# Performance work log

Hardware: AMD Instinct MI355X
Metric: run time of the kernel (lower is better)

## Reference

```python
import jax, jax.numpy as jnp
import numpy as np
import math

N_HEAD = 16
V_HEAD = 32   # v_head_dim
NOPE = 32     # nope_head_dim
ROPE_D = 64   # rope_head_dim
KEEP = 256    # num_tokens_to_keep
EPS = 1e-6


def _freqs(T, dim=ROPE_D, theta=10000.0):
    f = 1.0 / (theta ** (jnp.arange(0, dim, 2, dtype=jnp.float32) / dim))
    t = jnp.arange(T, dtype=jnp.float32)
    a = jnp.outer(t, f)  # [T, dim//2]
    return jnp.cos(a), jnp.sin(a)


def _rope(x, cos, sin):
    # x: [B,H,S,D]; half-split rotation as in apply_rope
    S = x.shape[-2]
    c = cos[:S][None, None]
    s = sin[:S][None, None]
    x1, x2 = jnp.split(x, 2, axis=-1)
    return jnp.concatenate([x1 * c - x2 * s, x1 * s + x2 * c], axis=-1)


def _rms(x, g, eps=EPS):
    return x * jax.lax.rsqrt(jnp.mean(x * x, axis=-1, keepdims=True) + eps) * g


def _attn(q, k, v, causal):
    scale = 1.0 / math.sqrt(q.shape[-1])
    s = jnp.einsum('bhqd,bhkd->bhqk', q, k) * scale
    if causal:
        Tq, Tk = s.shape[-2], s.shape[-1]
        mask = jnp.tril(jnp.ones((Tq, Tk), dtype=bool))
        s = jnp.where(mask, s, jnp.finfo(s.dtype).min)
    return jnp.einsum('bhqk,bhkd->bhqd', jax.nn.softmax(s, axis=-1), v)


def _forward(x, w_cq, g_qnorm, w_dq_nope, w_dq_rope, w_ckv, g_kvnorm,
             w_dk_nope, w_dv, w_krope, w_imp, w_selk, w_selv,
             w_wink, w_winv, w_gate, w_proj):
    B, T, C = x.shape
    cos, sin = _freqs(T)

    # --- MLA query path ---
    nq = _rms(x @ w_cq, g_qnorm)                                  # [B,T,96]
    q_nope = (nq @ w_dq_nope).reshape(B, T, N_HEAD, NOPE).transpose(0, 2, 1, 3)
    q_rope = (nq @ w_dq_rope).reshape(B, T, N_HEAD, ROPE_D).transpose(0, 2, 1, 3)
    q_rope = _rope(q_rope, cos, sin)
    q = jnp.concatenate([q_nope, q_rope], axis=-1)                # [B,H,T,96]

    # --- branch gate ---
    gate = jax.nn.softmax((x @ w_gate).mean(axis=1), axis=-1)     # [B,3]

    # --- branch 1: MLA-compressed full KV ---
    ckv = _rms(x @ w_ckv, g_kvnorm)                               # [B,T,32]
    k_nope = (ckv @ w_dk_nope).reshape(B, T, N_HEAD, NOPE).transpose(0, 2, 1, 3)
    v1 = (ckv @ w_dv).reshape(B, T, N_HEAD, V_HEAD).transpose(0, 2, 1, 3)
    k_rope = (x @ w_krope).reshape(B, T, 1, ROPE_D).transpose(0, 2, 1, 3) / N_HEAD
    k_rope = _rope(k_rope, cos, sin)
    k1 = jnp.concatenate(
        [k_nope, jnp.broadcast_to(k_rope, (B, N_HEAD, T, ROPE_D))], axis=-1)

    # --- branch 2: top-k selected tokens ---
    scores = (x @ w_imp)[..., 0]                                  # [B,T]
    _, idx = jax.lax.top_k(scores, KEEP)
    idx = jnp.sort(idx, axis=1)
    sel = jnp.take_along_axis(x, idx[:, :, None], axis=1)         # [B,S,C]
    ks = (sel @ w_selk).reshape(B, KEEP, N_HEAD, NOPE + ROPE_D).transpose(0, 2, 1, 3)
    vs = (sel @ w_selv).reshape(B, KEEP, N_HEAD, V_HEAD).transpose(0, 2, 1, 3)
    ks = jnp.concatenate([ks[..., :NOPE], _rope(ks[..., NOPE:], cos, sin)], axis=-1)

    # --- branch 3: sliding window (training mode -> full x) ---
    kw = (x @ w_wink).reshape(B, T, N_HEAD, NOPE + ROPE_D).transpose(0, 2, 1, 3)
    vw = (x @ w_winv).reshape(B, T, N_HEAD, V_HEAD).transpose(0, 2, 1, 3)
    kw = jnp.concatenate([kw[..., :NOPE], _rope(kw[..., NOPE:], cos, sin)], axis=-1)

    a1 = _attn(q, k1, v1, causal=True)
    a2 = _attn(q, ks, vs, causal=False)
    a3 = _attn(q, kw, vw, causal=True)

    g = gate[:, :, None, None, None]
    out = g[:, 0] * a1 + g[:, 1] * a2 + g[:, 2] * a3              # [B,H,T,Vd]
    out = out.transpose(0, 2, 1, 3).reshape(B, T, N_HEAD * V_HEAD)
    return out @ w_proj                                           # [B,T,C]


def setup_inputs() -> dict:
    key = jax.random.key(0)
    ks = jax.random.split(key, 20)
    B, T, C = 2, 1024, 1024
    q_lora, kv_lora = 96, 32
    std = 0.02
    def w(k, shape):
        return jax.random.normal(k, shape, dtype=jnp.float32) * std
    return {
        'x': jax.random.normal(ks[0], (B, T, C), dtype=jnp.float32),
        'w_cq': w(ks[1], (C, q_lora)),
        'g_qnorm': jnp.ones((q_lora,), jnp.float32),
        'w_dq_nope': w(ks[2], (q_lora, N_HEAD * NOPE)),
        'w_dq_rope': w(ks[3], (q_lora, N_HEAD * ROPE_D)),
        'w_ckv': w(ks[4], (C, kv_lora)),
        'g_kvnorm': jnp.ones((kv_lora,), jnp.float32),
        'w_dk_nope': w(ks[5], (kv_lora, N_HEAD * NOPE)),
        'w_dv': w(ks[6], (kv_lora, N_HEAD * V_HEAD)),
        'w_krope': w(ks[7], (C, ROPE_D)),
        'w_imp': w(ks[8], (C, 1)),
        'w_selk': w(ks[9], (C, N_HEAD * (NOPE + ROPE_D))),
        'w_selv': w(ks[10], (C, N_HEAD * V_HEAD)),
        'w_wink': w(ks[11], (C, N_HEAD * (NOPE + ROPE_D))),
        'w_winv': w(ks[12], (C, N_HEAD * V_HEAD)),
        'w_gate': w(ks[13], (C, 3)),
        'w_proj': w(ks[14], (N_HEAD * V_HEAD, C)),
    }


def reference(x, w_cq, g_qnorm, w_dq_nope, w_dq_rope, w_ckv, g_kvnorm,
              w_dk_nope, w_dv, w_krope, w_imp, w_selk, w_selv,
              w_wink, w_winv, w_gate, w_proj):
    return _forward(x, w_cq, g_qnorm, w_dq_nope, w_dq_rope, w_ckv, g_kvnorm,
                    w_dk_nope, w_dv, w_krope, w_imp, w_selk, w_selv,
                    w_wink, w_winv, w_gate, w_proj)
```

## Files before the change

kernel.cpp:

```cpp
#include <hip/hip_runtime.h>
#include <math.h>

#define T_SEQ   1024
#define BATCH   2
#define CDIM    1024
#define NHEAD   16
#define VHEAD   32
#define KEEP    256
#define HEAD_D  96
#define SCALE_ATTN 0.1020620726159658f

#define BQ   64
#define BKT  64
#define SK   100
#define SPT  66
#define SPV  36

#define GBK 16
#define SA  132

#define XWW    2244
#define C_CQ   0
#define C_CKV  96
#define C_KRO  128
#define C_WINK 192
#define C_WINV 1728
#define C_IMP  2240
#define C_GATE 2241

#define QKVW   2560
#define C_QN   0
#define C_QR   512
#define C_KN   1536
#define C_V1   2048

#define SKW  2048

__global__ __launch_bounds__(256) void gemm128(const float* __restrict__ A,
                                               const float* __restrict__ B,
                                               float* __restrict__ C,
                                               int M, int N, int K,
                                               int lda, int ldb, int ldc,
                                               int kchunk,
                                               const int* __restrict__ Arowidx,
                                               int rowdiv, int rowmul) {
    __shared__ float As[GBK][SA];
    __shared__ float Bs[GBK][SA];
    int t = threadIdx.x;
    int tx = t & 15, ty = t >> 4;
    int row0 = blockIdx.y * 128, col0 = blockIdx.x * 128;
    int kb = blockIdx.z * kchunk;
    int ke = min(K, kb + kchunk);
    float acc[8][8] = {};

    int asrc[2]; bool aok[2];
#pragma unroll
    for (int r = 0; r < 2; r++) {
        int idx = t + 256 * r;
        int row = idx >> 2;
        int gr = row0 + row;
        aok[r] = (gr < M);
        int ar = gr;
        if (Arowidx != nullptr && aok[r]) ar = (gr / rowdiv) * rowmul + Arowidx[gr];
        asrc[r] = ar;
    }

    for (int k0 = kb; k0 < ke; k0 += GBK) {
#pragma unroll
        for (int r = 0; r < 2; r++) {
            int idx = t + 256 * r;
            int row = idx >> 2, k4 = idx & 3;
            float4 v = make_float4(0.f, 0.f, 0.f, 0.f);
            if (aok[r]) v = *(const float4*)&A[(size_t)asrc[r] * lda + k0 + k4 * 4];
            As[k4 * 4 + 0][row] = v.x;
            As[k4 * 4 + 1][row] = v.y;
            As[k4 * 4 + 2][row] = v.z;
            As[k4 * 4 + 3][row] = v.w;
        }
#pragma unroll
        for (int r = 0; r < 2; r++) {
            int idx = t + 256 * r;
            int kk = idx >> 5, n4 = idx & 31;
            int gc = col0 + n4 * 4;
            float4 v = make_float4(0.f, 0.f, 0.f, 0.f);
            if (gc + 3 < N) {
                v = *(const float4*)&B[(size_t)(k0 + kk) * ldb + gc];
            } else if (gc < N) {
                const float* bp = &B[(size_t)(k0 + kk) * ldb];
                float tmp[4] = {0.f, 0.f, 0.f, 0.f};
                for (int j = 0; j < 4 && gc + j < N; j++) tmp[j] = bp[gc + j];
                v = make_float4(tmp[0], tmp[1], tmp[2], tmp[3]);
            }
            *(float4*)&Bs[kk][n4 * 4] = v;
        }
        __syncthreads();
#pragma unroll
        for (int kk = 0; kk < GBK; kk++) {
            float4 a0 = *(float4*)&As[kk][ty * 4];
            float4 a1 = *(float4*)&As[kk][64 + ty * 4];
            float4 b0 = *(float4*)&Bs[kk][tx * 4];
            float4 b1 = *(float4*)&Bs[kk][64 + tx * 4];
            float av[8] = {a0.x, a0.y, a0.z, a0.w, a1.x, a1.y, a1.z, a1.w};
            float bv[8] = {b0.x, b0.y, b0.z, b0.w, b1.x, b1.y, b1.z, b1.w};
#pragma unroll
            for (int i = 0; i < 8; i++)
#pragma unroll
                for (int j = 0; j < 8; j++) acc[i][j] += av[i] * bv[j];
        }
        __syncthreads();
    }

    bool split = (gridDim.z > 1);
#pragma unroll
    for (int i = 0; i < 8; i++) {
        int gr = row0 + ((i < 4) ? (ty * 4 + i) : (64 + ty * 4 + (i - 4)));
        if (gr >= M) continue;
#pragma unroll
        for (int half = 0; half < 2; half++) {
            int gc = col0 + half * 64 + tx * 4;
            if (gc + 3 >= N) continue;
            float* cp = &C[(size_t)gr * ldc + gc];
            if (split) {
                atomicAdd(cp + 0, acc[i][half * 4 + 0]);
                atomicAdd(cp + 1, acc[i][half * 4 + 1]);
                atomicAdd(cp + 2, acc[i][half * 4 + 2]);
                atomicAdd(cp + 3, acc[i][half * 4 + 3]);
            } else {
                *(float4*)cp = make_float4(acc[i][half * 4 + 0], acc[i][half * 4 + 1],
                                           acc[i][half * 4 + 2], acc[i][half * 4 + 3]);
            }
        }
    }
}

__global__ void pack_all(float* __restrict__ Bxw, float* __restrict__ Bqkv,
                         float* __restrict__ Bsel, float2* __restrict__ tab,
                         const float* __restrict__ cq, const float* __restrict__ ckv,
                         const float* __restrict__ kro, const float* __restrict__ wink,
                         const float* __restrict__ winv, const float* __restrict__ imp,
                         const float* __restrict__ gate,
                         const float* __restrict__ dqn, const float* __restrict__ dqr,
                         const float* __restrict__ dkn, const float* __restrict__ dv,
                         const float* __restrict__ selk, const float* __restrict__ selv) {
    int blk = blockIdx.x;
    if (blk < 1024) {
        int r = blk;
        for (int c = threadIdx.x; c < XWW; c += blockDim.x) {
            float v;
            if      (c < C_CKV)  v = cq  [(size_t)r * 96   + c];
            else if (c < C_KRO)  v = ckv [(size_t)r * 32   + (c - C_CKV)];
            else if (c < C_WINK) v = kro [(size_t)r * 64   + (c - C_KRO)];
            else if (c < C_WINV) v = wink[(size_t)r * 1536 + (c - C_WINK)];
            else if (c < C_IMP)  v = winv[(size_t)r * 512  + (c - C_WINV)];
            else if (c < C_GATE) v = imp [(size_t)r * 1    + (c - C_IMP)];
            else                 v = gate[(size_t)r * 3    + (c - C_GATE)];
            Bxw[(size_t)r * XWW + c] = v;
        }
    } else if (blk < 1152) {
        int r = blk - 1024;
        for (int c = threadIdx.x; c < QKVW; c += blockDim.x) {
            float v = 0.f;
            if (r < 96) {
                if (c < C_QR)      v = dqn[(size_t)r * 512 + c];
                else if (c < C_KN) v = dqr[(size_t)r * 1024 + (c - C_QR)];
            } else {
                if (c >= C_KN && c < C_V1) v = dkn[(size_t)(r - 96) * 512 + (c - C_KN)];
                else if (c >= C_V1)        v = dv [(size_t)(r - 96) * 512 + (c - C_V1)];
            }
            Bqkv[(size_t)r * QKVW + c] = v;
        }
    } else if (blk < 2176) {
        int r = blk - 1152;
        for (int c = threadIdx.x; c < SKW; c += blockDim.x) {
            float v = (c < 1536) ? selk[(size_t)r * 1536 + c]
                                 : selv[(size_t)r * 512 + (c - 1536)];
            Bsel[(size_t)r * SKW + c] = v;
        }
    } else {
        int idx = (blk - 2176) * 256 + threadIdx.x;
        if (idx < T_SEQ * 32) {
            int pos = idx >> 5, i = idx & 31;
            float expo = (float)i * (1.0f / 32.0f);
            float f = 1.0f / powf(10000.0f, expo);
            float a = (float)pos * f;
            float s, c;
            sincosf(a, &s, &c);
            tab[idx] = make_float2(c, s);
        }
    }
}

__global__ void xw_post(float* __restrict__ XW, const float* __restrict__ gq,
                        const float* __restrict__ gkv,
                        const float2* __restrict__ tab) {
    int row = blockIdx.x;
    int t = threadIdx.x;
    int w = t >> 6, lane = t & 63;
    float* rp = XW + (size_t)row * XWW;
    int pos = row & (T_SEQ - 1);
    const float2* tp = tab + pos * 32;

    if (w == 0) {
        float ss = 0.f;
        for (int d = lane; d < 96; d += 64) { float v = rp[d]; ss += v * v; }
        for (int off = 32; off; off >>= 1) ss += __shfl_xor(ss, off, 64);
        float r = rsqrtf(ss / 96.0f + 1e-6f);
        for (int d = lane; d < 96; d += 64) rp[d] *= r * gq[d];
    } else if (w == 1) {
        float ss = 0.f;
        for (int d = lane; d < 32; d += 64) { float v = rp[C_CKV + d]; ss += v * v; }
        for (int off = 32; off; off >>= 1) ss += __shfl_xor(ss, off, 64);
        float r = rsqrtf(ss / 32.0f + 1e-6f);
        for (int d = lane; d < 32; d += 64) rp[C_CKV + d] *= r * gkv[d];
    } else if (w == 2) {
        if (lane < 32) {
            float2 cs = tp[lane];
            float v1 = rp[C_KRO + lane], v2 = rp[C_KRO + 32 + lane];
            rp[C_KRO + lane]      = (v1 * cs.x - v2 * cs.y) * (1.0f / NHEAD);
            rp[C_KRO + 32 + lane] = (v1 * cs.y + v2 * cs.x) * (1.0f / NHEAD);
        }
    }
#pragma unroll
    for (int j = 0; j < 2; j++) {
        int item = t + j * 256;
        int h = item >> 5, i = item & 31;
        float2 cs = tp[i];
        size_t base = (size_t)(C_WINK + 32) + h * 96;
        float v1 = rp[base + i], v2 = rp[base + 32 + i];
        rp[base + i]      = v1 * cs.x - v2 * cs.y;
        rp[base + 32 + i] = v1 * cs.y + v2 * cs.x;
    }
}

__global__ void topk_gate(const float* __restrict__ xw, int* __restrict__ idx,
                          float* __restrict__ gate) {
    int b = blockIdx.x;
    __shared__ float s[1024];
    __shared__ int ps[1024];
    __shared__ float gred[3][16];
    int t = threadIdx.x;
    const float* rowp = &xw[((size_t)b * T_SEQ + t) * XWW];
    s[t] = rowp[C_IMP];
    float g0 = rowp[C_GATE + 0], g1 = rowp[C_GATE + 1], g2 = rowp[C_GATE + 2];
    for (int off = 32; off; off >>= 1) {
        g0 += __shfl_xor(g0, off, 64);
        g1 += __shfl_xor(g1, off, 64);
        g2 += __shfl_xor(g2, off, 64);
    }
    if ((t & 63) == 0) { int w = t >> 6; gred[0][w] = g0; gred[1][w] = g1; gred[2][w] = g2; }
    __syncthreads();
    if (t == 0) {
        float v0 = 0.f, v1 = 0.f, v2 = 0.f;
        for (int w = 0; w < 16; w++) { v0 += gred[0][w]; v1 += gred[1][w]; v2 += gred[2][w]; }
        v0 /= (float)T_SEQ; v1 /= (float)T_SEQ; v2 /= (float)T_SEQ;
        float m = fmaxf(v0, fmaxf(v1, v2));
        float e0 = expf(v0 - m), e1 = expf(v1 - m), e2 = expf(v2 - m);
        float ssum = e0 + e1 + e2;
        gate[b * 3 + 0] = e0 / ssum;
        gate[b * 3 + 1] = e1 / ssum;
        gate[b * 3 + 2] = e2 / ssum;
    }
    __syncthreads();
    float mine = s[t];
    int rank = 0;
    for (int j = 0; j < 1024; j++) {
        float v = s[j];
        rank += (v > mine) || (v == mine && j < t);
    }
    int selv = (rank < KEEP) ? 1 : 0;
    ps[t] = selv;
    __syncthreads();
    for (int off = 1; off < 1024; off <<= 1) {
        int add = (t >= off) ? ps[t - off] : 0;
        __syncthreads();
        ps[t] += add;
        __syncthreads();
    }
    if (selv) idx[b * KEEP + ps[t] - 1] = t;
}

__global__ __launch_bounds__(512, 4) void flash_fused(
    const float* __restrict__ qkv, const float* __restrict__ xw,
    const float* __restrict__ skv, const float* __restrict__ gate,
    const float2* __restrict__ tab, float* __restrict__ out) {
    __shared__ float Qs[BQ * SK];
    __shared__ float Ks[BKT * SK];
    __shared__ float Vs[BKT * SPV];
    __shared__ float Pt[BKT * SPT];

    int b = blockIdx.z, h = blockIdx.y;
    int qt = blockIdx.x;
    if (b == 1) qt = (gridDim.x - 1) - qt;
    int q0 = qt * BQ;
    int t = threadIdx.x;
    int tq = t >> 4, tk = t & 15;

    for (int i = t; i < BQ * 24; i += 512) {
        int row = i / 24, d4 = i % 24;
        size_t rq = (size_t)b * T_SEQ + q0 + row;
        float4 v;
        if (d4 < 8) {
            v = *(const float4*)&qkv[rq * QKVW + C_QN + h * 32 + d4 * 4];
        } else {
            const float* qb = &qkv[rq * QKVW + C_QR + h * 64];
            int dd = d4 - 8;
            float4 a = *(const float4*)&qb[dd * 4];
            const float2* tp = tab + (size_t)(q0 + row) * 32;
            if (dd < 8) {
                float4 p = *(const float4*)&qb[(dd + 8) * 4];
                int i0 = dd * 4;
                float2 c0 = tp[i0], c1 = tp[i0 + 1], c2 = tp[i0 + 2], c3 = tp[i0 + 3];
                v = make_float4(a.x * c0.x - p.x * c0.y, a.y * c1.x - p.y * c1.y,
                                a.z * c2.x - p.z * c2.y, a.w * c3.x - p.w * c3.y);
            } else {
                float4 p = *(const float4*)&qb[(dd - 8) * 4];
                int i0 = (dd - 8) * 4;
                float2 c0 = tp[i0], c1 = tp[i0 + 1], c2 = tp[i0 + 2], c3 = tp[i0 + 3];
                v = make_float4(p.x * c0.y + a.x * c0.x, p.y * c1.y + a.y * c1.x,
                                p.z * c2.y + a.z * c2.x, p.w * c3.y + a.w * c3.x);
            }
        }
        *(float4*)&Qs[row * SK + d4 * 4] = v;
    }

    int qq0 = q0 + 2 * tq, qq1 = qq0 + 1;
    float comb[2][2] = {};
    for (int phase = 0; phase < 3; phase++) {
        bool causal = (phase != 1);
        int ntiles = causal ? (qt + 1) : (KEEP / BKT);
        float m0 = -1e30f, m1 = -1e30f, l0 = 0.f, l1 = 0.f;
        float o00 = 0.f, o01 = 0.f, o10 = 0.f, o11 = 0.f;

        for (int kt = 0; kt < ntiles; kt++) {
            int j0 = kt * BKT;
            __syncthreads();

            for (int i = t; i < BKT * 24; i += 512) {
                int row = i / 24, d4 = i % 24;
                int j = j0 + row;
                float4 v;
                if (phase == 0) {
                    size_t rk = (size_t)b * T_SEQ + j;
                    if (d4 < 8) v = *(const float4*)&qkv[rk * QKVW + C_KN + h * 32 + d4 * 4];
                    else        v = *(const float4*)&xw[rk * XWW + C_KRO + (d4 - 8) * 4];
                } else if (phase == 1) {
                    const float* kb2 = &skv[((size_t)b * KEEP + j) * SKW + h * 96];
                    if (d4 < 8) {
                        v = *(const float4*)&kb2[d4 * 4];
                    } else {
                        int dd = d4 - 8;
                        float4 a = *(const float4*)&kb2[d4 * 4];
                        const float2* tp = tab + (size_t)j * 32;
                        if (dd < 8) {
                            float4 p = *(const float4*)&kb2[(d4 + 8) * 4];
                            int i0 = dd * 4;
                            float2 c0 = tp[i0], c1 = tp[i0 + 1], c2 = tp[i0 + 2], c3 = tp[i0 + 3];
                            v = make_float4(a.x * c0.x - p.x * c0.y, a.y * c1.x - p.y * c1.y,
                                            a.z * c2.x - p.z * c2.y, a.w * c3.x - p.w * c3.y);
                        } else {
                            float4 p = *(const float4*)&kb2[(d4 - 8) * 4];
                            int i0 = (dd - 8) * 4;
                            float2 c0 = tp[i0], c1 = tp[i0 + 1], c2 = tp[i0 + 2], c3 = tp[i0 + 3];
                            v = make_float4(p.x * c0.y + a.x * c0.x, p.y * c1.y + a.y * c1.x,
                                            p.z * c2.y + a.z * c2.x, p.w * c3.y + a.w * c3.x);
                        }
                    }
                } else {
                    v = *(const float4*)&xw[((size_t)b * T_SEQ + j) * XWW + C_WINK + h * 96 + d4 * 4];
                }
                *(float4*)&Ks[row * SK + d4 * 4] = v;
            }
            for (int i = t; i < BKT * 8; i += 512) {
                int row = i >> 3, d4 = i & 7;
                int j = j0 + row;
                float4 v;
                if (phase == 0)      v = *(const float4*)&qkv[((size_t)b * T_SEQ + j) * QKVW + C_V1 + h * 32 + d4 * 4];
                else if (phase == 1) v = *(const float4*)&skv[((size_t)b * KEEP  + j) * SKW + 1536 + h * 32 + d4 * 4];
                else                 v = *(const float4*)&xw[((size_t)b * T_SEQ + j) * XWW + C_WINV + h * 32 + d4 * 4];
                *(float4*)&Vs[row * SPV + d4 * 4] = v;
            }
            __syncthreads();

            float s0[4] = {}, s1[4] = {};
#pragma unroll 6
            for (int d = 0; d < HEAD_D; d += 4) {
                float4 qa = *(float4*)&Qs[(2 * tq)     * SK + d];
                float4 qb = *(float4*)&Qs[(2 * tq + 1) * SK + d];
#pragma unroll
                for (int j = 0; j < 4; j++) {
                    float4 kv = *(float4*)&Ks[(16 * j + tk) * SK + d];
                    s0[j] += qa.x * kv.x + qa.y * kv.y + qa.z * kv.z + qa.w * kv.w;
                    s1[j] += qb.x * kv.x + qb.y * kv.y + qb.z * kv.z + qb.w * kv.w;
                }
            }
            float mt0 = -1e30f, mt1 = -1e30f;
#pragma unroll
            for (int j = 0; j < 4; j++) {
                int kk = j0 + 16 * j + tk;
                s0[j] *= SCALE_ATTN;
                s1[j] *= SCALE_ATTN;
                if (causal && kk > qq0) s0[j] = -1e30f;
                if (causal && kk > qq1) s1[j] = -1e30f;
                mt0 = fmaxf(mt0, s0[j]);
                mt1 = fmaxf(mt1, s1[j]);
            }
#pragma unroll
            for (int off = 1; off <= 8; off <<= 1) {
                mt0 = fmaxf(mt0, __shfl_xor(mt0, off, 64));
                mt1 = fmaxf(mt1, __shfl_xor(mt1, off, 64));
            }
            float mn0 = fmaxf(m0, mt0), mn1 = fmaxf(m1, mt1);
            float a0 = __expf(m0 - mn0), a1 = __expf(m1 - mn1);
            m0 = mn0; m1 = mn1;

            float rs0 = 0.f, rs1 = 0.f;
#pragma unroll
            for (int j = 0; j < 4; j++) {
                float p0 = __expf(s0[j] - mn0);
                float p1 = __expf(s1[j] - mn1);
                rs0 += p0; rs1 += p1;
                *(float2*)&Pt[(16 * j + tk) * SPT + 2 * tq] = make_float2(p0, p1);
            }
#pragma unroll
            for (int off = 1; off <= 8; off <<= 1) {
                rs0 += __shfl_xor(rs0, off, 64);
                rs1 += __shfl_xor(rs1, off, 64);
            }
            l0 = l0 * a0 + rs0;
            l1 = l1 * a1 + rs1;

            o00 *= a0; o01 *= a0; o10 *= a1; o11 *= a1;
#pragma unroll 8
            for (int kk = 0; kk < BKT; kk++) {
                float2 pv = *(float2*)&Pt[kk * SPT + 2 * tq];
                float2 vv = *(float2*)&Vs[kk * SPV + 2 * tk];
                o00 += pv.x * vv.x; o01 += pv.x * vv.y;
                o10 += pv.y * vv.x; o11 += pv.y * vv.y;
            }
        }

        float g = gate[b * 3 + phase];
        float i0 = g / l0, i1 = g / l1;
        comb[0][0] += o00 * i0; comb[0][1] += o01 * i0;
        comb[1][0] += o10 * i1; comb[1][1] += o11 * i1;
    }

    size_t r0 = ((size_t)b * T_SEQ + q0 + 2 * tq) * 512 + h * 32 + 2 * tk;
    out[r0]           = comb[0][0];
    out[r0 + 1]       = comb[0][1];
    out[r0 + 512]     = comb[1][0];
    out[r0 + 512 + 1] = comb[1][1];
}

extern "C" void kernel_launch(void* const* d_in, const int* in_sizes, int n_in,
                              void* d_out, int out_size, void* d_ws, size_t ws_size,
                              hipStream_t stream) {
    const float* x        = (const float*)d_in[0];
    const float* w_cq     = (const float*)d_in[1];
    const float* g_qnorm  = (const float*)d_in[2];
    const float* w_dqn    = (const float*)d_in[3];
    const float* w_dqr    = (const float*)d_in[4];
    const float* w_ckv    = (const float*)d_in[5];
    const float* g_kvnorm = (const float*)d_in[6];
    const float* w_dkn    = (const float*)d_in[7];
    const float* w_dv     = (const float*)d_in[8];
    const float* w_krope  = (const float*)d_in[9];
    const float* w_imp    = (const float*)d_in[10];
    const float* w_selk   = (const float*)d_in[11];
    const float* w_selv   = (const float*)d_in[12];
    const float* w_wink   = (const float*)d_in[13];
    const float* w_winv   = (const float*)d_in[14];
    const float* w_gate   = (const float*)d_in[15];
    const float* w_proj   = (const float*)d_in[16];
    float* out = (float*)d_out;

    const int BT = BATCH * T_SEQ;
    const int BS = BATCH * KEEP;

    float* ws = (float*)d_ws;
    size_t o = 0;
    float* XW     = ws + o; o += (size_t)BT * XWW;
    float* QKV    = ws + o; o += (size_t)BT * QKVW;
    float* skv    = ws + o; o += (size_t)BS * SKW;
    float* attn   = ws + o; o += (size_t)BT * 512;
    float* Bxw    = ws + o; o += (size_t)CDIM * XWW;
    float* Bqkv   = ws + o; o += (size_t)128 * QKVW;
    float* Bsel   = ws + o; o += (size_t)CDIM * SKW;
    float2* tab   = (float2*)(ws + o); o += (size_t)T_SEQ * 32 * 2;
    float* gatef  = ws + o; o += 8;
    int*   idx    = (int*)(ws + o); o += 512;

    auto gemm = [&](const float* A, const float* Bm, float* C, int M, int N, int K,
                    int lda, int ldb, int ldc, int ksplit = 1,
                    const int* Arowidx = nullptr, int rowdiv = 1, int rowmul = 1) {
        int kchunk = (K / ksplit + GBK - 1) / GBK * GBK;
        dim3 grid((N + 127) / 128, (M + 127) / 128, ksplit);
        gemm128<<<grid, 256, 0, stream>>>(A, Bm, C, M, N, K, lda, ldb, ldc, kchunk,
                                          Arowidx, rowdiv, rowmul);
    };

    hipMemsetAsync(skv, 0, (size_t)BS * SKW * sizeof(float), stream);
    hipMemsetAsync(out, 0, (size_t)BT * CDIM * sizeof(float), stream);

    pack_all<<<2304, 256, 0, stream>>>(Bxw, Bqkv, Bsel, tab,
                                       w_cq, w_ckv, w_krope, w_wink, w_winv,
                                       w_imp, w_gate,
                                       w_dqn, w_dqr, w_dkn, w_dv, w_selk, w_selv);

    gemm(x, Bxw, XW, BT, XWW, CDIM, CDIM, XWW, XWW);

    xw_post<<<BT, 256, 0, stream>>>(XW, g_qnorm, g_kvnorm, tab);

    topk_gate<<<BATCH, 1024, 0, stream>>>(XW, idx, gatef);

    gemm(XW, Bqkv, QKV, BT, QKVW, 128, XWW, QKVW, QKVW);

    gemm(x, Bsel, skv, BS, SKW, CDIM, CDIM, SKW, SKW, 4, idx, KEEP, T_SEQ);

    dim3 fgrid(T_SEQ / BQ, NHEAD, BATCH);
    flash_fused<<<fgrid, 512, 0, stream>>>(QKV, XW, skv, gatef, tab, attn);

    gemm(attn, w_proj, out, BT, CDIM, 512, 512, CDIM, CDIM, 2);
}
```

Before: 953.7 us.

## Split-K the first projection GEMM, fold memsets into pack, pre-rotate selected keys

The large x·Bxw GEMM now uses a 4-way K split with atomic accumulation, which needs XW zeroed first. That zeroing, along with the skv and out zeroing, is folded into extra blocks of the pack kernel in place of separate memset calls. RoPE for the selected-branch keys moves out of the flash kernel's tile-load loop into a standalone rope_tab pass over skv, which simplifies the inner K loads. The trade-off is atomic traffic on a wide output, extra zero-fill bandwidth, and one more kernel launch.

```diff
diff --git a/kernel.cpp b/kernel.cpp
--- a/kernel.cpp
+++ b/kernel.cpp
@@ -135,6 +135,8 @@
 
 __global__ void pack_all(float* __restrict__ Bxw, float* __restrict__ Bqkv,
                          float* __restrict__ Bsel, float2* __restrict__ tab,
+                         float* __restrict__ XW, float* __restrict__ skv,
+                         float* __restrict__ outp,
                          const float* __restrict__ cq, const float* __restrict__ ckv,
                          const float* __restrict__ kro, const float* __restrict__ wink,
                          const float* __restrict__ winv, const float* __restrict__ imp,
@@ -176,7 +178,7 @@
                                  : selv[(size_t)r * 512 + (c - 1536)];
             Bsel[(size_t)r * SKW + c] = v;
         }
-    } else {
+    } else if (blk < 2304) {
         int idx = (blk - 2176) * 256 + threadIdx.x;
         if (idx < T_SEQ * 32) {
             int pos = idx >> 5, i = idx & 31;
@@ -187,6 +189,21 @@
             sincosf(a, &s, &c);
             tab[idx] = make_float2(c, s);
         }
+    } else if (blk < 3328) {
+        const size_t total4 = (size_t)BATCH * T_SEQ * XWW / 4;
+        for (size_t i = (size_t)(blk - 2304) * 256 + threadIdx.x; i < total4;
+             i += (size_t)1024 * 256)
+            ((float4*)XW)[i] = make_float4(0.f, 0.f, 0.f, 0.f);
+    } else if (blk < 3392) {
+        size_t base = (size_t)(blk - 3328) * 256 + threadIdx.x;
+#pragma unroll
+        for (int j = 0; j < 16; j++)
+            ((float4*)skv)[base + (size_t)j * 16384] = make_float4(0.f, 0.f, 0.f, 0.f);
+    } else {
+        size_t base = (size_t)(blk - 3392) * 256 + threadIdx.x;
+#pragma unroll
+        for (int j = 0; j < 16; j++)
+            ((float4*)outp)[base + (size_t)j * 32768] = make_float4(0.f, 0.f, 0.f, 0.f);
     }
 }
 
@@ -229,6 +246,25 @@
         float v1 = rp[base + i], v2 = rp[base + 32 + i];
         rp[base + i]      = v1 * cs.x - v2 * cs.y;
         rp[base + 32 + i] = v1 * cs.y + v2 * cs.x;
+    }
+}
+
+__global__ void rope_tab(float* __restrict__ buf, int nrows, int rstride,
+                         int nheads, int hstride, int roff, int posmod,
+                         const float2* __restrict__ tab) {
+    int total = nrows * nheads * 32;
+    for (int it = blockIdx.x * blockDim.x + threadIdx.x; it < total;
+         it += gridDim.x * blockDim.x) {
+        int i = it & 31;
+        int hr = it >> 5;
+        int h = hr % nheads;
+        int row = hr / nheads;
+        int pos = row % posmod;
+        float2 cs = tab[pos * 32 + i];
+        size_t base = (size_t)row * rstride + (size_t)h * hstride + roff;
+        float v1 = buf[base + i], v2 = buf[base + 32 + i];
+        buf[base + i]      = v1 * cs.x - v2 * cs.y;
+        buf[base + 32 + i] = v1 * cs.y + v2 * cs.x;
     }
 }
 
@@ -344,27 +380,7 @@
                     if (d4 < 8) v = *(const float4*)&qkv[rk * QKVW + C_KN + h * 32 + d4 * 4];
                     else        v = *(const float4*)&xw[rk * XWW + C_KRO + (d4 - 8) * 4];
                 } else if (phase == 1) {
-                    const float* kb2 = &skv[((size_t)b * KEEP + j) * SKW + h * 96];
-                    if (d4 < 8) {
-                        v = *(const float4*)&kb2[d4 * 4];
-                    } else {
-                        int dd = d4 - 8;
-                        float4 a = *(const float4*)&kb2[d4 * 4];
-                        const float2* tp = tab + (size_t)j * 32;
-                        if (dd < 8) {
-                            float4 p = *(const float4*)&kb2[(d4 + 8) * 4];
-                            int i0 = dd * 4;
-                            float2 c0 = tp[i0], c1 = tp[i0 + 1], c2 = tp[i0 + 2], c3 = tp[i0 + 3];
-                            v = make_float4(a.x * c0.x - p.x * c0.y, a.y * c1.x - p.y * c1.y,
-                                            a.z * c2.x - p.z * c2.y, a.w * c3.x - p.w * c3.y);
-                        } else {
-                            float4 p = *(const float4*)&kb2[(d4 - 8) * 4];
-                            int i0 = (dd - 8) * 4;
-                            float2 c0 = tp[i0], c1 = tp[i0 + 1], c2 = tp[i0 + 2], c3 = tp[i0 + 3];
-                            v = make_float4(p.x * c0.y + a.x * c0.x, p.y * c1.y + a.y * c1.x,
-                                            p.z * c2.y + a.z * c2.x, p.w * c3.y + a.w * c3.x);
-                        }
-                    }
+                    v = *(const float4*)&skv[((size_t)b * KEEP + j) * SKW + h * 96 + d4 * 4];
                 } else {
                     v = *(const float4*)&xw[((size_t)b * T_SEQ + j) * XWW + C_WINK + h * 96 + d4 * 4];
                 }
@@ -499,15 +515,12 @@
                                           Arowidx, rowdiv, rowmul);
     };
 
-    hipMemsetAsync(skv, 0, (size_t)BS * SKW * sizeof(float), stream);
-    hipMemsetAsync(out, 0, (size_t)BT * CDIM * sizeof(float), stream);
-
-    pack_all<<<2304, 256, 0, stream>>>(Bxw, Bqkv, Bsel, tab,
+    pack_all<<<3520, 256, 0, stream>>>(Bxw, Bqkv, Bsel, tab, XW, skv, out,
                                        w_cq, w_ckv, w_krope, w_wink, w_winv,
                                        w_imp, w_gate,
                                        w_dqn, w_dqr, w_dkn, w_dv, w_selk, w_selv);
 
-    gemm(x, Bxw, XW, BT, XWW, CDIM, CDIM, XWW, XWW);
+    gemm(x, Bxw, XW, BT, XWW, CDIM, CDIM, XWW, XWW, 4);
 
     xw_post<<<BT, 256, 0, stream>>>(XW, g_qnorm, g_kvnorm, tab);
 
@@ -516,6 +529,7 @@
     gemm(XW, Bqkv, QKV, BT, QKVW, 128, XWW, QKVW, QKVW);
 
     gemm(x, Bsel, skv, BS, SKW, CDIM, CDIM, SKW, SKW, 4, idx, KEEP, T_SEQ);
+    rope_tab<<<512, 256, 0, stream>>>(skv, BS, SKW, 16, 96, 32, KEEP, tab);
 
     dim3 fgrid(T_SEQ / BQ, NHEAD, BATCH);
     flash_fused<<<fgrid, 512, 0, stream>>>(QKV, XW, skv, gatef, tab, attn);
```

New measurement: 1.104 ms. +15.8%, slower.
